# Optimization experiments

Measured on AMD Instinct MI355X. Metric: run time of the kernel, lower is better.

The kernel has to match this reference:

```python
import jax, jax.numpy as jnp
import numpy as np

N_NODES = 100000
N_EDGES = 800000
N_LABEL = 400000
IN_CH = 256
OUT_CH = 256
H1 = 128
H2 = 32


def setup_inputs() -> dict:
    key = jax.random.key(0)
    ks = jax.random.split(key, 12)
    x = jax.random.normal(ks[0], (N_NODES, IN_CH), dtype=jnp.float32)
    edge_index = jax.random.randint(ks[1], (2, N_EDGES), 0, N_NODES, dtype=jnp.int64)
    edge_label_index = jax.random.randint(ks[2], (2, N_LABEL), 0, N_NODES, dtype=jnp.int64)
    # GCNConv params (PyG: lin weight + bias)
    s = 1.0 / np.sqrt(IN_CH)
    W_gcn = jax.random.uniform(ks[3], (IN_CH, OUT_CH), minval=-s, maxval=s, dtype=jnp.float32)
    b_gcn = jnp.zeros((OUT_CH,), dtype=jnp.float32)
    def lin(kw, kb, fin, fout):
        bound = 1.0 / np.sqrt(fin)
        W = jax.random.uniform(kw, (fin, fout), minval=-bound, maxval=bound, dtype=jnp.float32)
        b = jax.random.uniform(kb, (fout,), minval=-bound, maxval=bound, dtype=jnp.float32)
        return W, b
    W1, b1 = lin(ks[4], ks[5], OUT_CH, H1)
    W2, b2 = lin(ks[6], ks[7], H1, H2)
    W3, b3 = lin(ks[8], ks[9], H2, 1)
    return {"x": x, "edge_index": edge_index, "edge_label_index": edge_label_index,
            "W_gcn": W_gcn, "b_gcn": b_gcn, "W1": W1, "b1": b1,
            "W2": W2, "b2": b2, "W3": W3, "b3": b3}


def _gcn_conv(x, edge_index, W, b):
    # x' = D^{-1/2} (A + I) D^{-1/2} (x W) + b   (PyG GCNConv defaults)
    n = x.shape[0]
    x = x @ W  # [N, out]
    loops = jnp.arange(n, dtype=edge_index.dtype)
    src = jnp.concatenate([edge_index[0], loops])  # messages flow src -> dst
    dst = jnp.concatenate([edge_index[1], loops])
    deg = jax.ops.segment_sum(jnp.ones_like(dst, dtype=x.dtype), dst, num_segments=n)
    dis = jnp.where(deg > 0, jax.lax.rsqrt(jnp.maximum(deg, 1.0)), 0.0)
    norm = dis[src] * dis[dst]  # [E+N]
    msgs = x[src] * norm[:, None]
    out = jax.ops.segment_sum(msgs, dst, num_segments=n)
    return out + b


def reference(x, edge_index, edge_label_index, W_gcn, b_gcn, W1, b1, W2, b2, W3, b3):
    h = _gcn_conv(x, edge_index, W_gcn, b_gcn)  # [N, out]
    d = h[edge_label_index[1]] - h[edge_label_index[0]]  # [E_q, out]
    d = jax.nn.relu(d @ W1 + b1)
    d = jax.nn.relu(d @ W2 + b2)
    prob = d @ W3 + b3  # [E_q, 1]
    return prob.reshape(-1)
```

## Files before the change

kernel.cpp:

```cpp
#include <hip/hip_runtime.h>

#define N_NODES 100000
#define N_EDGES 800000
#define N_LABEL 400000

typedef __attribute__((ext_vector_type(8))) short bf16x8;
typedef __attribute__((ext_vector_type(4))) float f32x4;
typedef unsigned int uint;
typedef unsigned short ushort;

__device__ __forceinline__ ushort f2bf(float f) {
    uint u = __float_as_uint(f);
    u += 0x7FFFu + ((u >> 16) & 1u);
    return (ushort)(u >> 16);
}
__device__ __forceinline__ uint pack2(ushort a, ushort b) {
    return (uint)a | ((uint)b << 16);
}

__global__ void k_zero2(int* __restrict__ a, int* __restrict__ b) {
    int i = blockIdx.x * 256 + threadIdx.x;
    if (i < N_NODES) { a[i] = 0; b[i] = 0; }
}

__global__ void k_count(const int* __restrict__ ei, int* __restrict__ cnt) {
    int e = blockIdx.x * 256 + threadIdx.x;
    if (e < N_EDGES) atomicAdd(&cnt[ei[N_EDGES + e]], 1);
}

__global__ void k_dis(const int* __restrict__ cnt, float* __restrict__ dis) {
    int i = blockIdx.x * 256 + threadIdx.x;
    if (i < N_NODES) dis[i] = rsqrtf((float)(cnt[i] + 1));
}

__global__ __launch_bounds__(1024) void k_bsum(const int* __restrict__ cnt,
                                               int* __restrict__ bsum) {
    __shared__ int red[1024];
    int t = threadIdx.x;
    int i = blockIdx.x * 1024 + t;
    red[t] = (i < N_NODES) ? cnt[i] : 0;
    __syncthreads();
    #pragma unroll
    for (int off = 512; off; off >>= 1) {
        if (t < off) red[t] += red[t + off];
        __syncthreads();
    }
    if (t == 0) bsum[blockIdx.x] = red[0];
}

__global__ void k_bscan(int* __restrict__ bsum, int nb) {
    __shared__ int s[128];
    int t = threadIdx.x;
    s[t] = (t < nb) ? bsum[t] : 0;
    __syncthreads();
    #pragma unroll
    for (int off = 1; off < 128; off <<= 1) {
        int v = (t >= off) ? s[t - off] : 0;
        __syncthreads();
        s[t] += v;
        __syncthreads();
    }
    if (t < nb) bsum[t] = t ? s[t - 1] : 0;
}

__global__ __launch_bounds__(1024) void k_rowptr(const int* __restrict__ cnt,
                                                 const int* __restrict__ bsum,
                                                 int* __restrict__ rowptr) {
    __shared__ int s[1024];
    int t = threadIdx.x;
    int i = blockIdx.x * 1024 + t;
    int v = (i < N_NODES) ? cnt[i] : 0;
    s[t] = v;
    __syncthreads();
    #pragma unroll
    for (int off = 1; off < 1024; off <<= 1) {
        int u = (t >= off) ? s[t - off] : 0;
        __syncthreads();
        s[t] += u;
        __syncthreads();
    }
    int excl = s[t] - v + bsum[blockIdx.x];
    if (i < N_NODES) rowptr[i] = excl;
    if (i == N_NODES - 1) rowptr[N_NODES] = excl + v;
}

__global__ void k_fill(const int* __restrict__ ei, const int* __restrict__ rowptr,
                       int* __restrict__ cursor, int* __restrict__ csr) {
    int e = blockIdx.x * 256 + threadIdx.x;
    if (e >= N_EDGES) return;
    int src = ei[e];
    int dst = ei[N_EDGES + e];
    int pos = rowptr[dst] + atomicAdd(&cursor[dst], 1);
    csr[pos] = src;
}

__global__ __launch_bounds__(256) void gemm_f32(
    const float* __restrict__ A, const float* __restrict__ B,
    float* __restrict__ C, int M, int N, int K,
    const float* __restrict__ rowscale) {
    __shared__ float As[2][16][132];
    __shared__ float Bs[2][16][132];

    const int tid = threadIdx.x;
    const int tx = tid & 15, ty = tid >> 4;
    const int m0 = blockIdx.x * 128, n0 = blockIdx.y * 128;

    const int ar = tid >> 2;
    const int ac = (tid & 3) * 4;
    const int bk = tid >> 5;
    const int bc = (tid & 31) * 4;

    float acc[8][8] = {};
    float4 va[2], vb[2];

    auto loadG = [&](int k0) {
        #pragma unroll
        for (int hh = 0; hh < 2; ++hh) {
            int row = m0 + ar + hh * 64;
            va[hh] = make_float4(0.f, 0.f, 0.f, 0.f);
            if (row < M) va[hh] = *(const float4*)&A[(size_t)row * K + k0 + ac];
            vb[hh] = *(const float4*)&B[(size_t)(k0 + bk + hh * 8) * N + n0 + bc];
        }
    };
    auto storeL = [&](int buf) {
        #pragma unroll
        for (int hh = 0; hh < 2; ++hh) {
            As[buf][ac + 0][ar + hh * 64] = va[hh].x;
            As[buf][ac + 1][ar + hh * 64] = va[hh].y;
            As[buf][ac + 2][ar + hh * 64] = va[hh].z;
            As[buf][ac + 3][ar + hh * 64] = va[hh].w;
            *(float4*)&Bs[buf][bk + hh * 8][bc] = vb[hh];
        }
    };

    loadG(0);
    storeL(0);
    __syncthreads();

    int cur = 0;
    for (int k0 = 16;; k0 += 16) {
        const bool last = (k0 >= K);
        if (!last) loadG(k0);

        #pragma unroll
        for (int kk = 0; kk < 16; ++kk) {
            const float4 a0 = *(const float4*)&As[cur][kk][ty * 8];
            const float4 a1 = *(const float4*)&As[cur][kk][ty * 8 + 4];
            const float4 b0 = *(const float4*)&Bs[cur][kk][tx * 8];
            const float4 b1 = *(const float4*)&Bs[cur][kk][tx * 8 + 4];
            const float aa[8] = {a0.x, a0.y, a0.z, a0.w, a1.x, a1.y, a1.z, a1.w};
            const float bb[8] = {b0.x, b0.y, b0.z, b0.w, b1.x, b1.y, b1.z, b1.w};
            #pragma unroll
            for (int i = 0; i < 8; ++i)
                #pragma unroll
                for (int j = 0; j < 8; ++j)
                    acc[i][j] = fmaf(aa[i], bb[j], acc[i][j]);
        }
        if (last) break;
        storeL(cur ^ 1);
        __syncthreads();
        cur ^= 1;
    }

    #pragma unroll
    for (int i = 0; i < 8; ++i) {
        int row = m0 + ty * 8 + i;
        if (row < M) {
            float s = rowscale ? rowscale[row] : 1.0f;
            float4 c0 = {acc[i][0] * s, acc[i][1] * s, acc[i][2] * s, acc[i][3] * s};
            float4 c1 = {acc[i][4] * s, acc[i][5] * s, acc[i][6] * s, acc[i][7] * s};
            *(float4*)&C[(size_t)row * N + n0 + tx * 8] = c0;
            *(float4*)&C[(size_t)row * N + n0 + tx * 8 + 4] = c1;
        }
    }
}

__global__ void k_wsplit(const float* __restrict__ Wf, ushort* __restrict__ Bh,
                         ushort* __restrict__ Bl) {
    int id = blockIdx.x * 256 + threadIdx.x;
    if (id >= 32768) return;
    int j = id & 7, l = (id >> 3) & 63, ct = (id >> 9) & 7, s = id >> 12;
    int k = s * 32 + (l >> 4) * 8 + j;
    int col = ct * 16 + (l & 15);
    float w = Wf[k * 128 + col];
    ushort h = f2bf(w);
    float hf = __uint_as_float(((uint)h) << 16);
    ushort lo = f2bf(w - hf);
    Bh[id] = h;
    Bl[id] = lo;
}

__global__ void k_w2split(const float* __restrict__ W2, ushort* __restrict__ W2h,
                          ushort* __restrict__ W2l) {
    int id = blockIdx.x * 256 + threadIdx.x;
    if (id >= 4096) return;
    int j = id & 7, l = (id >> 3) & 63, ct = (id >> 9) & 1, s = id >> 10;
    int k = s * 32 + (l >> 4) * 8 + j;
    int col = ct * 16 + (l & 15);
    float w = W2[k * 32 + col];
    ushort h = f2bf(w);
    float hf = __uint_as_float(((uint)h) << 16);
    ushort lo = f2bf(w - hf);
    W2h[id] = h;
    W2l[id] = lo;
}

__global__ __launch_bounds__(256) void gemm_mfma(
    const float* __restrict__ x, const ushort* __restrict__ Bh,
    const ushort* __restrict__ Bl, const float* __restrict__ dis,
    float* __restrict__ qs) {
    __shared__ __align__(16) ushort Ah[4096], Al[4096], Bhs[4096], Bls[4096];

    const int tid = threadIdx.x;
    const int w = tid >> 6, lane = tid & 63;
    const int m0 = blockIdx.x * 128;
    const int srow = tid >> 3;
    const int skq = tid & 7;

    f32x4 acc[2][8];
    #pragma unroll
    for (int i = 0; i < 2; ++i)
        #pragma unroll
        for (int j = 0; j < 8; ++j)
            acc[i][j] = (f32x4){0.f, 0.f, 0.f, 0.f};

    float4 r0, r1, r2, r3;
    uint4 pb0, pb1, pc0, pc1;

    auto xload = [&](int s) {
        const int kc = s * 32 + skq * 4;
        int row;
        const float4 z = make_float4(0.f, 0.f, 0.f, 0.f);
        row = m0 + srow;       r0 = (row < N_NODES) ? *(const float4*)&x[(size_t)row * 256 + kc] : z;
        row = m0 + 32 + srow;  r1 = (row < N_NODES) ? *(const float4*)&x[(size_t)row * 256 + kc] : z;
        row = m0 + 64 + srow;  r2 = (row < N_NODES) ? *(const float4*)&x[(size_t)row * 256 + kc] : z;
        row = m0 + 96 + srow;  r3 = (row < N_NODES) ? *(const float4*)&x[(size_t)row * 256 + kc] : z;
    };
    auto bload = [&](int s) {
        const uint4* ph = (const uint4*)(Bh + s * 4096);
        const uint4* pl = (const uint4*)(Bl + s * 4096);
        pb0 = ph[tid * 2]; pb1 = ph[tid * 2 + 1];
        pc0 = pl[tid * 2]; pc1 = pl[tid * 2 + 1];
    };
    auto stageA = [&](int p, const float4& v) {
        const int off = ((p * 2 + (srow >> 4)) * 64 + (skq >> 1) * 16 + (srow & 15)) * 8
                        + (skq & 1) * 4;
        ushort h0 = f2bf(v.x), h1 = f2bf(v.y), h2 = f2bf(v.z), h3 = f2bf(v.w);
        *(uint2*)&Ah[off] = make_uint2(pack2(h0, h1), pack2(h2, h3));
        float l0 = v.x - __uint_as_float(((uint)h0) << 16);
        float l1 = v.y - __uint_as_float(((uint)h1) << 16);
        float l2 = v.z - __uint_as_float(((uint)h2) << 16);
        float l3 = v.w - __uint_as_float(((uint)h3) << 16);
        *(uint2*)&Al[off] = make_uint2(pack2(f2bf(l0), f2bf(l1)),
                                       pack2(f2bf(l2), f2bf(l3)));
    };

    xload(0);
    bload(0);

    for (int s = 0; s < 8; ++s) {
        if (s) __syncthreads();
        stageA(0, r0); stageA(1, r1); stageA(2, r2); stageA(3, r3);
        *(uint4*)&Bhs[tid * 16] = pb0; *(uint4*)&Bhs[tid * 16 + 8] = pb1;
        *(uint4*)&Bls[tid * 16] = pc0; *(uint4*)&Bls[tid * 16 + 8] = pc1;
        if (s < 7) { xload(s + 1); bload(s + 1); }
        __syncthreads();

        const bf16x8 ah0 = *(const bf16x8*)&Ah[((w * 2 + 0) * 64 + lane) * 8];
        const bf16x8 al0 = *(const bf16x8*)&Al[((w * 2 + 0) * 64 + lane) * 8];
        const bf16x8 ah1 = *(const bf16x8*)&Ah[((w * 2 + 1) * 64 + lane) * 8];
        const bf16x8 al1 = *(const bf16x8*)&Al[((w * 2 + 1) * 64 + lane) * 8];
        #pragma unroll
        for (int ct = 0; ct < 8; ++ct) {
            const bf16x8 bh = *(const bf16x8*)&Bhs[(ct * 64 + lane) * 8];
            const bf16x8 bl = *(const bf16x8*)&Bls[(ct * 64 + lane) * 8];
            acc[0][ct] = __builtin_amdgcn_mfma_f32_16x16x32_bf16(al0, bh, acc[0][ct], 0, 0, 0);
            acc[0][ct] = __builtin_amdgcn_mfma_f32_16x16x32_bf16(ah0, bl, acc[0][ct], 0, 0, 0);
            acc[0][ct] = __builtin_amdgcn_mfma_f32_16x16x32_bf16(ah0, bh, acc[0][ct], 0, 0, 0);
            acc[1][ct] = __builtin_amdgcn_mfma_f32_16x16x32_bf16(al1, bh, acc[1][ct], 0, 0, 0);
            acc[1][ct] = __builtin_amdgcn_mfma_f32_16x16x32_bf16(ah1, bl, acc[1][ct], 0, 0, 0);
            acc[1][ct] = __builtin_amdgcn_mfma_f32_16x16x32_bf16(ah1, bh, acc[1][ct], 0, 0, 0);
        }
    }

    #pragma unroll
    for (int rt = 0; rt < 2; ++rt) {
        #pragma unroll
        for (int j = 0; j < 4; ++j) {
            const int row = m0 + w * 32 + rt * 16 + (lane >> 4) * 4 + j;
            if (row < N_NODES) {
                const float sc = dis[row];
                #pragma unroll
                for (int ct = 0; ct < 8; ++ct)
                    qs[(size_t)row * 128 + ct * 16 + (lane & 15)] = acc[rt][ct][j] * sc;
            }
        }
    }
}

__global__ __launch_bounds__(256) void k_gather(
    const float* __restrict__ qs, const int* __restrict__ rowptr,
    const int* __restrict__ csr, const float* __restrict__ dis,
    float* __restrict__ p) {
    int node = blockIdx.x * 4 + (threadIdx.x >> 6);
    if (node >= N_NODES) return;
    int lane = threadIdx.x & 63;
    int beg = rowptr[node], end = rowptr[node + 1];
    float2 acc = *(const float2*)&qs[(size_t)node * 128 + lane * 2];
    int j = beg;
    for (; j + 8 <= end; j += 8) {
        int s0 = csr[j],     s1 = csr[j + 1], s2 = csr[j + 2], s3 = csr[j + 3];
        int s4 = csr[j + 4], s5 = csr[j + 5], s6 = csr[j + 6], s7 = csr[j + 7];
        float2 v0 = *(const float2*)&qs[(size_t)s0 * 128 + lane * 2];
        float2 v1 = *(const float2*)&qs[(size_t)s1 * 128 + lane * 2];
        float2 v2 = *(const float2*)&qs[(size_t)s2 * 128 + lane * 2];
        float2 v3 = *(const float2*)&qs[(size_t)s3 * 128 + lane * 2];
        float2 v4 = *(const float2*)&qs[(size_t)s4 * 128 + lane * 2];
        float2 v5 = *(const float2*)&qs[(size_t)s5 * 128 + lane * 2];
        float2 v6 = *(const float2*)&qs[(size_t)s6 * 128 + lane * 2];
        float2 v7 = *(const float2*)&qs[(size_t)s7 * 128 + lane * 2];
        acc.x += v0.x; acc.y += v0.y;  acc.x += v1.x; acc.y += v1.y;
        acc.x += v2.x; acc.y += v2.y;  acc.x += v3.x; acc.y += v3.y;
        acc.x += v4.x; acc.y += v4.y;  acc.x += v5.x; acc.y += v5.y;
        acc.x += v6.x; acc.y += v6.y;  acc.x += v7.x; acc.y += v7.y;
    }
    for (; j + 4 <= end; j += 4) {
        int s0 = csr[j], s1 = csr[j + 1], s2 = csr[j + 2], s3 = csr[j + 3];
        float2 v0 = *(const float2*)&qs[(size_t)s0 * 128 + lane * 2];
        float2 v1 = *(const float2*)&qs[(size_t)s1 * 128 + lane * 2];
        float2 v2 = *(const float2*)&qs[(size_t)s2 * 128 + lane * 2];
        float2 v3 = *(const float2*)&qs[(size_t)s3 * 128 + lane * 2];
        acc.x += v0.x; acc.y += v0.y;  acc.x += v1.x; acc.y += v1.y;
        acc.x += v2.x; acc.y += v2.y;  acc.x += v3.x; acc.y += v3.y;
    }
    for (; j < end; ++j) {
        int src = csr[j];
        float2 v = *(const float2*)&qs[(size_t)src * 128 + lane * 2];
        acc.x += v.x;
        acc.y += v.y;
    }
    float d = dis[node];
    float2 r = {acc.x * d, acc.y * d};
    *(float2*)&p[(size_t)node * 128 + lane * 2] = r;
}

__global__ __launch_bounds__(256, 4) void k_edge_mlp(
    const float* __restrict__ p, const int* __restrict__ eli,
    const float* __restrict__ b1, const ushort* __restrict__ W2h,
    const ushort* __restrict__ W2l, const float* __restrict__ b2,
    const float* __restrict__ W3, const float* __restrict__ b3,
    float* __restrict__ out) {
    __shared__ __align__(16) ushort sth[4][2048], stl[4][2048];

    const int tid = threadIdx.x;
    const int wave = tid >> 6, lane = tid & 63;
    const int row = lane & 15;
    const int s = lane >> 4;

    const int e0 = (blockIdx.x * 4 + wave) * 16;
    const int src = eli[e0 + row];
    const int dst = eli[N_LABEL + e0 + row];
    const float* prd = &p[(size_t)dst * 128 + s * 32];
    const float* prs = &p[(size_t)src * 128 + s * 32];

    bf16x8 w2h[4][2], w2l[4][2];
    #pragma unroll
    for (int ss = 0; ss < 4; ++ss)
        #pragma unroll
        for (int ct = 0; ct < 2; ++ct) {
            w2h[ss][ct] = *(const bf16x8*)&W2h[((ss * 2 + ct) * 64 + lane) * 8];
            w2l[ss][ct] = *(const bf16x8*)&W2l[((ss * 2 + ct) * 64 + lane) * 8];
        }

    #pragma unroll
    for (int cc = 0; cc < 8; ++cc) {
        const float4 pd = *(const float4*)&prd[cc * 4];
        const float4 ps = *(const float4*)&prs[cc * 4];
        const float4 bb = *(const float4*)&b1[s * 32 + cc * 4];
        float t0 = fmaxf(pd.x - ps.x + bb.x, 0.f);
        float t1 = fmaxf(pd.y - ps.y + bb.y, 0.f);
        float t2 = fmaxf(pd.z - ps.z + bb.z, 0.f);
        float t3 = fmaxf(pd.w - ps.w + bb.w, 0.f);
        ushort h0 = f2bf(t0), h1 = f2bf(t1), h2 = f2bf(t2), h3 = f2bf(t3);
        const int off = (s * 64 + (cc >> 1) * 16 + row) * 8 + (cc & 1) * 4;
        *(uint2*)&sth[wave][off] = make_uint2(pack2(h0, h1), pack2(h2, h3));
        float l0 = t0 - __uint_as_float(((uint)h0) << 16);
        float l1 = t1 - __uint_as_float(((uint)h1) << 16);
        float l2 = t2 - __uint_as_float(((uint)h2) << 16);
        float l3 = t3 - __uint_as_float(((uint)h3) << 16);
        *(uint2*)&stl[wave][off] = make_uint2(pack2(f2bf(l0), f2bf(l1)),
                                              pack2(f2bf(l2), f2bf(l3)));
    }

    f32x4 acc[2];
    acc[0] = (f32x4){0.f, 0.f, 0.f, 0.f};
    acc[1] = (f32x4){0.f, 0.f, 0.f, 0.f};
    #pragma unroll
    for (int ss = 0; ss < 4; ++ss) {
        const bf16x8 ah = *(const bf16x8*)&sth[wave][(ss * 64 + lane) * 8];
        const bf16x8 al = *(const bf16x8*)&stl[wave][(ss * 64 + lane) * 8];
        #pragma unroll
        for (int ct = 0; ct < 2; ++ct) {
            acc[ct] = __builtin_amdgcn_mfma_f32_16x16x32_bf16(al, w2h[ss][ct], acc[ct], 0, 0, 0);
            acc[ct] = __builtin_amdgcn_mfma_f32_16x16x32_bf16(ah, w2l[ss][ct], acc[ct], 0, 0, 0);
            acc[ct] = __builtin_amdgcn_mfma_f32_16x16x32_bf16(ah, w2h[ss][ct], acc[ct], 0, 0, 0);
        }
    }

    const float b2a = b2[lane & 15];
    const float b2b = b2[16 + (lane & 15)];
    const float w3a = W3[lane & 15];
    const float w3b = W3[16 + (lane & 15)];
    const float b3r = b3[0];
    #pragma unroll
    for (int j = 0; j < 4; ++j) {
        float v = fmaxf(acc[0][j] + b2a, 0.f) * w3a
                + fmaxf(acc[1][j] + b2b, 0.f) * w3b;
        v += __shfl_xor(v, 1);
        v += __shfl_xor(v, 2);
        v += __shfl_xor(v, 4);
        v += __shfl_xor(v, 8);
        if ((lane & 15) == 0) out[e0 + s * 4 + j] = v + b3r;
    }
}

extern "C" void kernel_launch(void* const* d_in, const int* in_sizes, int n_in,
                              void* d_out, int out_size, void* d_ws, size_t ws_size,
                              hipStream_t stream) {
    const float* x   = (const float*)d_in[0];
    const int*   ei  = (const int*)d_in[1];
    const int*   eli = (const int*)d_in[2];
    const float* Wg  = (const float*)d_in[3];
    const float* W1  = (const float*)d_in[5];
    const float* b1  = (const float*)d_in[6];
    const float* W2  = (const float*)d_in[7];
    const float* b2  = (const float*)d_in[8];
    const float* W3  = (const float*)d_in[9];
    const float* b3  = (const float*)d_in[10];
    float* out = (float*)d_out;

    char* ws = (char*)d_ws;
    float*  dis    = (float*)(ws + 0);
    int*    cnt    = (int*)(ws + 524288);
    int*    cursor = (int*)(ws + 1048576);
    int*    rowptr = (int*)(ws + 1572864);
    int*    bsum   = (int*)(ws + 2000000);
    int*    csr    = (int*)(ws + 2097152);
    float*  Wf     = (float*)(ws + 6291456);
    ushort* Bh     = (ushort*)(ws + 6422528);
    ushort* Bl     = (ushort*)(ws + 6488064);
    ushort* W2h    = (ushort*)(ws + 6553600);
    ushort* W2l    = (ushort*)(ws + 6561792);
    float*  qs     = (float*)(ws + 8388608);
    float*  p      = (float*)(ws + 59588608);

    const int NB = (N_NODES + 1023) / 1024;

    k_zero2<<<(N_NODES + 255) / 256, 256, 0, stream>>>(cnt, cursor);
    k_count<<<(N_EDGES + 255) / 256, 256, 0, stream>>>(ei, cnt);
    k_dis<<<(N_NODES + 255) / 256, 256, 0, stream>>>(cnt, dis);
    k_bsum<<<NB, 1024, 0, stream>>>(cnt, bsum);
    k_bscan<<<1, 128, 0, stream>>>(bsum, NB);
    k_rowptr<<<NB, 1024, 0, stream>>>(cnt, bsum, rowptr);
    k_fill<<<(N_EDGES + 255) / 256, 256, 0, stream>>>(ei, rowptr, cursor, csr);

    gemm_f32<<<dim3(2, 1), 256, 0, stream>>>(Wg, W1, Wf, 256, 128, 256, nullptr);

    k_wsplit<<<128, 256, 0, stream>>>(Wf, Bh, Bl);
    k_w2split<<<16, 256, 0, stream>>>(W2, W2h, W2l);

    gemm_mfma<<<(N_NODES + 127) / 128, 256, 0, stream>>>(x, Bh, Bl, dis, qs);

    k_gather<<<(N_NODES + 3) / 4, 256, 0, stream>>>(qs, rowptr, csr, dis, p);

    k_edge_mlp<<<N_LABEL / 64, 256, 0, stream>>>(p, eli, b1, W2h, W2l, b2, W3, b3, out);
}
```

Measured before the change: 344.0 us.

## Fold degree rsqrt into rowptr scan and pipeline edge MLP over multiple tiles

Removes the separate k_dis launch by computing the inverse-sqrt degree inside the rowptr scan kernel. The edge MLP kernel now processes four 16-edge tiles per wave instead of one, staging the split W2 weights once per block in LDS. It double-buffers the gathered p rows so the next tile's global loads overlap the current tile's MFMA work. The trade-off is extra LDS use and register pressure from the double buffers, plus LDS reads of W2 in place of register-resident weights.

```diff
diff --git a/kernel.cpp b/kernel.cpp
--- a/kernel.cpp
+++ b/kernel.cpp
@@ -26,11 +26,6 @@
 __global__ void k_count(const int* __restrict__ ei, int* __restrict__ cnt) {
     int e = blockIdx.x * 256 + threadIdx.x;
     if (e < N_EDGES) atomicAdd(&cnt[ei[N_EDGES + e]], 1);
-}
-
-__global__ void k_dis(const int* __restrict__ cnt, float* __restrict__ dis) {
-    int i = blockIdx.x * 256 + threadIdx.x;
-    if (i < N_NODES) dis[i] = rsqrtf((float)(cnt[i] + 1));
 }
 
 __global__ __launch_bounds__(1024) void k_bsum(const int* __restrict__ cnt,
@@ -65,7 +60,8 @@
 
 __global__ __launch_bounds__(1024) void k_rowptr(const int* __restrict__ cnt,
                                                  const int* __restrict__ bsum,
-                                                 int* __restrict__ rowptr) {
+                                                 int* __restrict__ rowptr,
+                                                 float* __restrict__ dis) {
     __shared__ int s[1024];
     int t = threadIdx.x;
     int i = blockIdx.x * 1024 + t;
@@ -80,7 +76,10 @@
         __syncthreads();
     }
     int excl = s[t] - v + bsum[blockIdx.x];
-    if (i < N_NODES) rowptr[i] = excl;
+    if (i < N_NODES) {
+        rowptr[i] = excl;
+        dis[i] = rsqrtf((float)(v + 1));
+    }
     if (i == N_NODES - 1) rowptr[N_NODES] = excl + v;
 }
 
@@ -351,76 +350,101 @@
     const float* __restrict__ W3, const float* __restrict__ b3,
     float* __restrict__ out) {
     __shared__ __align__(16) ushort sth[4][2048], stl[4][2048];
+    __shared__ __align__(16) ushort w2hs[4096], w2ls[4096];
 
     const int tid = threadIdx.x;
     const int wave = tid >> 6, lane = tid & 63;
     const int row = lane & 15;
     const int s = lane >> 4;
 
-    const int e0 = (blockIdx.x * 4 + wave) * 16;
-    const int src = eli[e0 + row];
-    const int dst = eli[N_LABEL + e0 + row];
-    const float* prd = &p[(size_t)dst * 128 + s * 32];
-    const float* prs = &p[(size_t)src * 128 + s * 32];
-
-    bf16x8 w2h[4][2], w2l[4][2];
-    #pragma unroll
-    for (int ss = 0; ss < 4; ++ss)
-        #pragma unroll
-        for (int ct = 0; ct < 2; ++ct) {
-            w2h[ss][ct] = *(const bf16x8*)&W2h[((ss * 2 + ct) * 64 + lane) * 8];
-            w2l[ss][ct] = *(const bf16x8*)&W2l[((ss * 2 + ct) * 64 + lane) * 8];
-        }
-
-    #pragma unroll
-    for (int cc = 0; cc < 8; ++cc) {
-        const float4 pd = *(const float4*)&prd[cc * 4];
-        const float4 ps = *(const float4*)&prs[cc * 4];
-        const float4 bb = *(const float4*)&b1[s * 32 + cc * 4];
-        float t0 = fmaxf(pd.x - ps.x + bb.x, 0.f);
-        float t1 = fmaxf(pd.y - ps.y + bb.y, 0.f);
-        float t2 = fmaxf(pd.z - ps.z + bb.z, 0.f);
-        float t3 = fmaxf(pd.w - ps.w + bb.w, 0.f);
-        ushort h0 = f2bf(t0), h1 = f2bf(t1), h2 = f2bf(t2), h3 = f2bf(t3);
-        const int off = (s * 64 + (cc >> 1) * 16 + row) * 8 + (cc & 1) * 4;
-        *(uint2*)&sth[wave][off] = make_uint2(pack2(h0, h1), pack2(h2, h3));
-        float l0 = t0 - __uint_as_float(((uint)h0) << 16);
-        float l1 = t1 - __uint_as_float(((uint)h1) << 16);
-        float l2 = t2 - __uint_as_float(((uint)h2) << 16);
-        float l3 = t3 - __uint_as_float(((uint)h3) << 16);
-        *(uint2*)&stl[wave][off] = make_uint2(pack2(f2bf(l0), f2bf(l1)),
-                                              pack2(f2bf(l2), f2bf(l3)));
-    }
-
-    f32x4 acc[2];
-    acc[0] = (f32x4){0.f, 0.f, 0.f, 0.f};
-    acc[1] = (f32x4){0.f, 0.f, 0.f, 0.f};
-    #pragma unroll
-    for (int ss = 0; ss < 4; ++ss) {
-        const bf16x8 ah = *(const bf16x8*)&sth[wave][(ss * 64 + lane) * 8];
-        const bf16x8 al = *(const bf16x8*)&stl[wave][(ss * 64 + lane) * 8];
-        #pragma unroll
-        for (int ct = 0; ct < 2; ++ct) {
-            acc[ct] = __builtin_amdgcn_mfma_f32_16x16x32_bf16(al, w2h[ss][ct], acc[ct], 0, 0, 0);
-            acc[ct] = __builtin_amdgcn_mfma_f32_16x16x32_bf16(ah, w2l[ss][ct], acc[ct], 0, 0, 0);
-            acc[ct] = __builtin_amdgcn_mfma_f32_16x16x32_bf16(ah, w2h[ss][ct], acc[ct], 0, 0, 0);
-        }
-    }
-
-    const float b2a = b2[lane & 15];
-    const float b2b = b2[16 + (lane & 15)];
-    const float w3a = W3[lane & 15];
-    const float w3b = W3[16 + (lane & 15)];
+    *(uint4*)&w2hs[tid * 16]     = *(const uint4*)&W2h[tid * 16];
+    *(uint4*)&w2hs[tid * 16 + 8] = *(const uint4*)&W2h[tid * 16 + 8];
+    *(uint4*)&w2ls[tid * 16]     = *(const uint4*)&W2l[tid * 16];
+    *(uint4*)&w2ls[tid * 16 + 8] = *(const uint4*)&W2l[tid * 16 + 8];
+    __syncthreads();
+
+    const int e0 = (blockIdx.x * 4 + wave) * 64;
+
+    int srcs[4], dsts[4];
+    #pragma unroll
+    for (int b = 0; b < 4; ++b) {
+        const int eb = (e0 + b * 16 < N_LABEL) ? e0 + b * 16 : 0;
+        srcs[b] = eli[eb + row];
+        dsts[b] = eli[N_LABEL + eb + row];
+    }
+
+    const float b2a = b2[row];
+    const float b2b = b2[16 + row];
+    const float w3a = W3[row];
+    const float w3b = W3[16 + row];
     const float b3r = b3[0];
-    #pragma unroll
-    for (int j = 0; j < 4; ++j) {
-        float v = fmaxf(acc[0][j] + b2a, 0.f) * w3a
-                + fmaxf(acc[1][j] + b2b, 0.f) * w3b;
-        v += __shfl_xor(v, 1);
-        v += __shfl_xor(v, 2);
-        v += __shfl_xor(v, 4);
-        v += __shfl_xor(v, 8);
-        if ((lane & 15) == 0) out[e0 + s * 4 + j] = v + b3r;
+
+    float4 pdb[2][8], psb[2][8];
+    auto loadrows = [&](int b, int buf) {
+        const float* prd = &p[(size_t)dsts[b] * 128 + s * 32];
+        const float* prs = &p[(size_t)srcs[b] * 128 + s * 32];
+        #pragma unroll
+        for (int cc = 0; cc < 8; ++cc) {
+            pdb[buf][cc] = *(const float4*)&prd[cc * 4];
+            psb[buf][cc] = *(const float4*)&prs[cc * 4];
+        }
+    };
+
+    loadrows(0, 0);
+
+    #pragma unroll
+    for (int b = 0; b < 4; ++b) {
+        const int cur = b & 1;
+        #pragma unroll
+        for (int cc = 0; cc < 8; ++cc) {
+            const float4 pd = pdb[cur][cc];
+            const float4 ps = psb[cur][cc];
+            const float4 bb = *(const float4*)&b1[s * 32 + cc * 4];
+            float t0 = fmaxf(pd.x - ps.x + bb.x, 0.f);
+            float t1 = fmaxf(pd.y - ps.y + bb.y, 0.f);
+            float t2 = fmaxf(pd.z - ps.z + bb.z, 0.f);
+            float t3 = fmaxf(pd.w - ps.w + bb.w, 0.f);
+            ushort h0 = f2bf(t0), h1 = f2bf(t1), h2 = f2bf(t2), h3 = f2bf(t3);
+            const int off = (s * 64 + (cc >> 1) * 16 + row) * 8 + (cc & 1) * 4;
+            *(uint2*)&sth[wave][off] = make_uint2(pack2(h0, h1), pack2(h2, h3));
+            float l0 = t0 - __uint_as_float(((uint)h0) << 16);
+            float l1 = t1 - __uint_as_float(((uint)h1) << 16);
+            float l2 = t2 - __uint_as_float(((uint)h2) << 16);
+            float l3 = t3 - __uint_as_float(((uint)h3) << 16);
+            *(uint2*)&stl[wave][off] = make_uint2(pack2(f2bf(l0), f2bf(l1)),
+                                                  pack2(f2bf(l2), f2bf(l3)));
+        }
+        if (b < 3) loadrows(b + 1, cur ^ 1);
+
+        f32x4 acc0 = (f32x4){0.f, 0.f, 0.f, 0.f};
+        f32x4 acc1 = (f32x4){0.f, 0.f, 0.f, 0.f};
+        #pragma unroll
+        for (int ss = 0; ss < 4; ++ss) {
+            const bf16x8 ah = *(const bf16x8*)&sth[wave][(ss * 64 + lane) * 8];
+            const bf16x8 al = *(const bf16x8*)&stl[wave][(ss * 64 + lane) * 8];
+            const bf16x8 bh0 = *(const bf16x8*)&w2hs[((ss * 2 + 0) * 64 + lane) * 8];
+            const bf16x8 bl0 = *(const bf16x8*)&w2ls[((ss * 2 + 0) * 64 + lane) * 8];
+            const bf16x8 bh1 = *(const bf16x8*)&w2hs[((ss * 2 + 1) * 64 + lane) * 8];
+            const bf16x8 bl1 = *(const bf16x8*)&w2ls[((ss * 2 + 1) * 64 + lane) * 8];
+            acc0 = __builtin_amdgcn_mfma_f32_16x16x32_bf16(al, bh0, acc0, 0, 0, 0);
+            acc0 = __builtin_amdgcn_mfma_f32_16x16x32_bf16(ah, bl0, acc0, 0, 0, 0);
+            acc0 = __builtin_amdgcn_mfma_f32_16x16x32_bf16(ah, bh0, acc0, 0, 0, 0);
+            acc1 = __builtin_amdgcn_mfma_f32_16x16x32_bf16(al, bh1, acc1, 0, 0, 0);
+            acc1 = __builtin_amdgcn_mfma_f32_16x16x32_bf16(ah, bl1, acc1, 0, 0, 0);
+            acc1 = __builtin_amdgcn_mfma_f32_16x16x32_bf16(ah, bh1, acc1, 0, 0, 0);
+        }
+
+        const bool wr = (e0 + b * 16) < N_LABEL;
+        #pragma unroll
+        for (int j = 0; j < 4; ++j) {
+            float v = fmaxf(acc0[j] + b2a, 0.f) * w3a
+                    + fmaxf(acc1[j] + b2b, 0.f) * w3b;
+            v += __shfl_xor(v, 1);
+            v += __shfl_xor(v, 2);
+            v += __shfl_xor(v, 4);
+            v += __shfl_xor(v, 8);
+            if (wr && row == 0) out[e0 + b * 16 + s * 4 + j] = v + b3r;
+        }
     }
 }
 
@@ -458,10 +482,9 @@
 
     k_zero2<<<(N_NODES + 255) / 256, 256, 0, stream>>>(cnt, cursor);
     k_count<<<(N_EDGES + 255) / 256, 256, 0, stream>>>(ei, cnt);
-    k_dis<<<(N_NODES + 255) / 256, 256, 0, stream>>>(cnt, dis);
     k_bsum<<<NB, 1024, 0, stream>>>(cnt, bsum);
     k_bscan<<<1, 128, 0, stream>>>(bsum, NB);
-    k_rowptr<<<NB, 1024, 0, stream>>>(cnt, bsum, rowptr);
+    k_rowptr<<<NB, 1024, 0, stream>>>(cnt, bsum, rowptr, dis);
     k_fill<<<(N_EDGES + 255) / 256, 256, 0, stream>>>(ei, rowptr, cursor, csr);
 
     gemm_f32<<<dim3(2, 1), 256, 0, stream>>>(Wg, W1, Wf, 256, 128, 256, nullptr);
@@ -473,5 +496,6 @@
 
     k_gather<<<(N_NODES + 3) / 4, 256, 0, stream>>>(qs, rowptr, csr, dis, p);
 
-    k_edge_mlp<<<N_LABEL / 64, 256, 0, stream>>>(p, eli, b1, W2h, W2l, b2, W3, b3, out);
-}
+    k_edge_mlp<<<(N_LABEL / 16 + 15) / 16, 256, 0, stream>>>(
+        p, eli, b1, W2h, W2l, b2, W3, b3, out);
+}
```

Result: faster. 330.7 us (-3.9%).
